# Kernel optimization log

Measured on AMD Instinct MI355X. Metric: run time of the kernel, lower is better.

## Reference

```python
import jax, jax.numpy as jnp
import numpy as np

# STDPConfig defaults
A_PLUS = 0.01
A_MINUS = 0.012
TAU_PLUS = 0.02
TAU_MINUS = 0.02
W_MIN = 0.0
W_MAX = 1.0
MAX_DT = 0.1
NEG_INF = -1e9  # stands in for -inf initial last-spike times (avoids inf-inf NaNs)


def setup_inputs() -> dict:
    key = jax.random.key(0)
    k1, k2, k3 = jax.random.split(key, 3)
    B, P, Q = 16, 2048, 2048
    pre_spikes = jax.random.bernoulli(k1, 0.05, (B, P)).astype(jnp.float32)
    post_spikes = jax.random.bernoulli(k2, 0.05, (B, Q)).astype(jnp.float32)
    # module initializes weights to a constant; randomize in [w_min, w_max] for a stronger test
    weights = jax.random.uniform(k3, (P, Q), jnp.float32, W_MIN, W_MAX)
    pre_trace = jnp.zeros((B, P), jnp.float32)
    post_trace = jnp.zeros((B, Q), jnp.float32)
    last_pre_spike = jnp.full((B, P), NEG_INF, jnp.float32)
    last_post_spike = jnp.full((B, Q), NEG_INF, jnp.float32)
    return {
        'pre_spikes': pre_spikes,
        'post_spikes': post_spikes,
        'weights': weights,
        'pre_trace': pre_trace,
        'post_trace': post_trace,
        'last_pre_spike': last_pre_spike,
        'last_post_spike': last_post_spike,
        'current_time': 0.5,
        'dt': 0.001,
    }


def reference(pre_spikes, post_spikes, weights, pre_trace, post_trace,
              last_pre_spike, last_post_spike, current_time, dt):
    # --- update last spike times ---
    pre_mask = pre_spikes > 0    # [B, P]
    post_mask = post_spikes > 0  # [B, Q]
    t_pre = jnp.where(pre_mask, current_time, last_pre_spike)    # [B, P]
    t_post = jnp.where(post_mask, current_time, last_post_spike)  # [B, Q]

    # --- trace decay + accumulation ---
    pre_trace_new = pre_trace * jnp.exp(jnp.float32(-dt / TAU_PLUS)) + pre_spikes
    post_trace_new = post_trace * jnp.exp(jnp.float32(-dt / TAU_MINUS)) + post_spikes

    # --- synaptic transmission ---
    synaptic_current = jnp.matmul(pre_spikes, weights)  # [B, Q]

    # --- vectorized STDP pairwise update (replaces the triple loop) ---
    # pair (i, j) is active iff pre i spiked AND post j spiked this step
    pair = pre_mask[:, :, None] & post_mask[:, None, :]              # [B, P, Q]
    dts = t_post[:, None, :] - t_pre[:, :, None]                     # post_time - pre_time
    dts = jnp.where(pair, dts, 0.0)                                  # mask out garbage (-inf diffs)
    ltp_cond = pair & (dts > 0) & (dts <= MAX_DT)
    ltd_cond = pair & (dts < 0) & (-dts <= MAX_DT)
    ltp = jnp.where(ltp_cond, A_PLUS * jnp.exp(-dts / TAU_PLUS), 0.0)
    ltd = jnp.where(ltd_cond, -A_MINUS * jnp.exp(dts / TAU_MINUS), 0.0)
    weight_changes = (ltp + ltd).mean(axis=0)                        # [P, Q]

    # --- multiplicative soft-bound update ---
    pot_change = weight_changes * (W_MAX - weights)
    dep_change = weight_changes * (weights - W_MIN)
    weight_update = jnp.where(weight_changes > 0, pot_change, dep_change)
    new_weights = jnp.clip(weights + weight_update, W_MIN, W_MAX)

    return (synaptic_current, weight_changes, pre_trace_new, post_trace_new, new_weights)
```

## Files before the change

kernel.cpp:

```cpp
#include <hip/hip_runtime.h>
#include <math.h>

#define B     16
#define PDIM  2048
#define QDIM  2048

#define NQB    8
#define NPC    64
#define PCHUNK 32

__global__ __launch_bounds__(256) void stdp_main(
    const float* __restrict__ pre_spikes,
    const float* __restrict__ weights,
    float* __restrict__ nw,
    float* __restrict__ wc,
    float* __restrict__ ws)
{
    __shared__ float sp[PCHUNK][B];

    const int qb   = blockIdx.x & (NQB - 1);
    const int pc   = blockIdx.x >> 3;
    const int p0   = pc * PCHUNK;
    const int wave = threadIdx.x >> 6;
    const int lane = threadIdx.x & 63;
    const int q    = qb * 256 + lane * 4;
    const int b0   = wave * 4;

    for (int t = threadIdx.x; t < B * PCHUNK; t += 256) {
        const int b  = t >> 5;
        const int pl = t & (PCHUNK - 1);
        sp[pl][b] = pre_spikes[b * PDIM + p0 + pl];
    }
    __syncthreads();

    float4 acc0 = {0,0,0,0}, acc1 = {0,0,0,0}, acc2 = {0,0,0,0}, acc3 = {0,0,0,0};

    const size_t base = (size_t)p0 * QDIM + q;
    const float* __restrict__ wp  = weights + base;
    float* __restrict__       nwp = nw + base;
    float* __restrict__       wcp = wc + base;

    #pragma unroll 8
    for (int i = 0; i < PCHUNK; ++i) {
        const float4 w = *(const float4*)(wp + (size_t)i * QDIM);
        const float4 s = *(const float4*)&sp[i][b0];

        acc0.x = fmaf(s.x, w.x, acc0.x); acc0.y = fmaf(s.x, w.y, acc0.y);
        acc0.z = fmaf(s.x, w.z, acc0.z); acc0.w = fmaf(s.x, w.w, acc0.w);
        acc1.x = fmaf(s.y, w.x, acc1.x); acc1.y = fmaf(s.y, w.y, acc1.y);
        acc1.z = fmaf(s.y, w.z, acc1.z); acc1.w = fmaf(s.y, w.w, acc1.w);
        acc2.x = fmaf(s.z, w.x, acc2.x); acc2.y = fmaf(s.z, w.y, acc2.y);
        acc2.z = fmaf(s.z, w.z, acc2.z); acc2.w = fmaf(s.z, w.w, acc2.w);
        acc3.x = fmaf(s.w, w.x, acc3.x); acc3.y = fmaf(s.w, w.y, acc3.y);
        acc3.z = fmaf(s.w, w.z, acc3.z); acc3.w = fmaf(s.w, w.w, acc3.w);

        if (wave == 0) {
            float4 c;
            c.x = fminf(fmaxf(w.x, 0.0f), 1.0f);
            c.y = fminf(fmaxf(w.y, 0.0f), 1.0f);
            c.z = fminf(fmaxf(w.z, 0.0f), 1.0f);
            c.w = fminf(fmaxf(w.w, 0.0f), 1.0f);
            *(float4*)(nwp + (size_t)i * QDIM) = c;
        } else if (wave == 1) {
            const float4 z = {0,0,0,0};
            *(float4*)(wcp + (size_t)i * QDIM) = z;
        }
    }

    float* __restrict__ wsp = ws + ((size_t)(pc * B + b0)) * QDIM + q;
    *(float4*)(wsp + 0 * (size_t)QDIM) = acc0;
    *(float4*)(wsp + 1 * (size_t)QDIM) = acc1;
    *(float4*)(wsp + 2 * (size_t)QDIM) = acc2;
    *(float4*)(wsp + 3 * (size_t)QDIM) = acc3;
}

__global__ __launch_bounds__(256) void stdp_tail(
    const float* __restrict__ pre_s,
    const float* __restrict__ post_s,
    const float* __restrict__ pre_t,
    const float* __restrict__ post_t,
    const float* __restrict__ dtp,
    const float* __restrict__ ws,
    float* __restrict__ pre_o,
    float* __restrict__ post_o,
    float* __restrict__ sc)
{
    const int i = blockIdx.x * blockDim.x + threadIdx.x;
    const float decay = expf(-dtp[0] * 50.0f);
    pre_o[i]  = pre_t[i]  * decay + pre_s[i];
    post_o[i] = post_t[i] * decay + post_s[i];

    if (i < (B * QDIM) / 4) {
        const int b  = i >> 9;
        const int qc = (i & 511) << 2;
        const float* __restrict__ p = ws + (size_t)b * QDIM + qc;
        float4 s = {0,0,0,0};
        #pragma unroll 8
        for (int pc = 0; pc < NPC; ++pc) {
            const float4 v = *(const float4*)(p + (size_t)pc * B * QDIM);
            s.x += v.x; s.y += v.y; s.z += v.z; s.w += v.w;
        }
        *(float4*)(sc + (size_t)b * QDIM + qc) = s;
    }
}

extern "C" void kernel_launch(void* const* d_in, const int* in_sizes, int n_in,
                              void* d_out, int out_size, void* d_ws, size_t ws_size,
                              hipStream_t stream) {
    const float* pre_spikes  = (const float*)d_in[0];
    const float* post_spikes = (const float*)d_in[1];
    const float* weights     = (const float*)d_in[2];
    const float* pre_trace   = (const float*)d_in[3];
    const float* post_trace  = (const float*)d_in[4];
    const float* dtp         = (const float*)d_in[8];

    float* out    = (float*)d_out;
    float* sc     = out;
    float* wc     = out + (size_t)B * QDIM;
    float* pre_o  = wc  + (size_t)PDIM * QDIM;
    float* post_o = pre_o + (size_t)B * PDIM;
    float* nw     = post_o + (size_t)B * QDIM;

    float* ws = (float*)d_ws;

    stdp_main<<<dim3(NQB * NPC), dim3(256), 0, stream>>>(
        pre_spikes, weights, nw, wc, ws);

    stdp_tail<<<dim3((B * PDIM) / 256), dim3(256), 0, stream>>>(
        pre_spikes, post_spikes, pre_trace, post_trace, dtp, ws, pre_o, post_o, sc);
}
```

Before: 101.9 us.

## Fuse trace update into main kernel and halve partial-sum chunks

```diff
diff --git a/kernel.cpp b/kernel.cpp
--- a/kernel.cpp
+++ b/kernel.cpp
@@ -6,15 +6,21 @@
 #define QDIM  2048
 
 #define NQB    8
-#define NPC    64
-#define PCHUNK 32
+#define NPC    32
+#define PCHUNK 64
 
-__global__ __launch_bounds__(256) void stdp_main(
+__global__ __launch_bounds__(512) void stdp_main(
     const float* __restrict__ pre_spikes,
+    const float* __restrict__ post_spikes,
+    const float* __restrict__ pre_trace,
+    const float* __restrict__ post_trace,
+    const float* __restrict__ dtp,
     const float* __restrict__ weights,
     float* __restrict__ nw,
     float* __restrict__ wc,
-    float* __restrict__ ws)
+    float* __restrict__ ws,
+    float* __restrict__ pre_o,
+    float* __restrict__ post_o)
 {
     __shared__ float sp[PCHUNK][B];
 
@@ -24,16 +30,39 @@
     const int wave = threadIdx.x >> 6;
     const int lane = threadIdx.x & 63;
     const int q    = qb * 256 + lane * 4;
-    const int b0   = wave * 4;
+    const int b0   = wave * 2;
 
-    for (int t = threadIdx.x; t < B * PCHUNK; t += 256) {
-        const int b  = t >> 5;
+    {
+        const int t = blockIdx.x * 512 + threadIdx.x;
+        if (t < 16384) {
+            const float decay = expf(-dtp[0] * 50.0f);
+            if (t < 8192) {
+                const float4 s = ((const float4*)pre_spikes)[t];
+                const float4 r = ((const float4*)pre_trace)[t];
+                float4 o;
+                o.x = fmaf(r.x, decay, s.x); o.y = fmaf(r.y, decay, s.y);
+                o.z = fmaf(r.z, decay, s.z); o.w = fmaf(r.w, decay, s.w);
+                ((float4*)pre_o)[t] = o;
+            } else {
+                const int u = t - 8192;
+                const float4 s = ((const float4*)post_spikes)[u];
+                const float4 r = ((const float4*)post_trace)[u];
+                float4 o;
+                o.x = fmaf(r.x, decay, s.x); o.y = fmaf(r.y, decay, s.y);
+                o.z = fmaf(r.z, decay, s.z); o.w = fmaf(r.w, decay, s.w);
+                ((float4*)post_o)[u] = o;
+            }
+        }
+    }
+
+    for (int t = threadIdx.x; t < B * PCHUNK; t += 512) {
+        const int b  = t >> 6;
         const int pl = t & (PCHUNK - 1);
         sp[pl][b] = pre_spikes[b * PDIM + p0 + pl];
     }
     __syncthreads();
 
-    float4 acc0 = {0,0,0,0}, acc1 = {0,0,0,0}, acc2 = {0,0,0,0}, acc3 = {0,0,0,0};
+    float4 acc0 = {0,0,0,0}, acc1 = {0,0,0,0};
 
     const size_t base = (size_t)p0 * QDIM + q;
     const float* __restrict__ wp  = weights + base;
@@ -43,16 +72,12 @@
     #pragma unroll 8
     for (int i = 0; i < PCHUNK; ++i) {
         const float4 w = *(const float4*)(wp + (size_t)i * QDIM);
-        const float4 s = *(const float4*)&sp[i][b0];
+        const float2 s = *(const float2*)&sp[i][b0];
 
         acc0.x = fmaf(s.x, w.x, acc0.x); acc0.y = fmaf(s.x, w.y, acc0.y);
         acc0.z = fmaf(s.x, w.z, acc0.z); acc0.w = fmaf(s.x, w.w, acc0.w);
         acc1.x = fmaf(s.y, w.x, acc1.x); acc1.y = fmaf(s.y, w.y, acc1.y);
         acc1.z = fmaf(s.y, w.z, acc1.z); acc1.w = fmaf(s.y, w.w, acc1.w);
-        acc2.x = fmaf(s.z, w.x, acc2.x); acc2.y = fmaf(s.z, w.y, acc2.y);
-        acc2.z = fmaf(s.z, w.z, acc2.z); acc2.w = fmaf(s.z, w.w, acc2.w);
-        acc3.x = fmaf(s.w, w.x, acc3.x); acc3.y = fmaf(s.w, w.y, acc3.y);
-        acc3.z = fmaf(s.w, w.z, acc3.z); acc3.w = fmaf(s.w, w.w, acc3.w);
 
         if (wave == 0) {
             float4 c;
@@ -70,38 +95,23 @@
     float* __restrict__ wsp = ws + ((size_t)(pc * B + b0)) * QDIM + q;
     *(float4*)(wsp + 0 * (size_t)QDIM) = acc0;
     *(float4*)(wsp + 1 * (size_t)QDIM) = acc1;
-    *(float4*)(wsp + 2 * (size_t)QDIM) = acc2;
-    *(float4*)(wsp + 3 * (size_t)QDIM) = acc3;
 }
 
-__global__ __launch_bounds__(256) void stdp_tail(
-    const float* __restrict__ pre_s,
-    const float* __restrict__ post_s,
-    const float* __restrict__ pre_t,
-    const float* __restrict__ post_t,
-    const float* __restrict__ dtp,
+__global__ __launch_bounds__(64) void stdp_screduce(
     const float* __restrict__ ws,
-    float* __restrict__ pre_o,
-    float* __restrict__ post_o,
     float* __restrict__ sc)
 {
-    const int i = blockIdx.x * blockDim.x + threadIdx.x;
-    const float decay = expf(-dtp[0] * 50.0f);
-    pre_o[i]  = pre_t[i]  * decay + pre_s[i];
-    post_o[i] = post_t[i] * decay + post_s[i];
-
-    if (i < (B * QDIM) / 4) {
-        const int b  = i >> 9;
-        const int qc = (i & 511) << 2;
-        const float* __restrict__ p = ws + (size_t)b * QDIM + qc;
-        float4 s = {0,0,0,0};
-        #pragma unroll 8
-        for (int pc = 0; pc < NPC; ++pc) {
-            const float4 v = *(const float4*)(p + (size_t)pc * B * QDIM);
-            s.x += v.x; s.y += v.y; s.z += v.z; s.w += v.w;
-        }
-        *(float4*)(sc + (size_t)b * QDIM + qc) = s;
+    const int u  = blockIdx.x * 64 + threadIdx.x;
+    const int b  = u >> 9;
+    const int qc = (u & 511) << 2;
+    const float* __restrict__ p = ws + (size_t)b * QDIM + qc;
+    float4 s = {0,0,0,0};
+    #pragma unroll
+    for (int pc = 0; pc < NPC; ++pc) {
+        const float4 v = *(const float4*)(p + (size_t)pc * B * QDIM);
+        s.x += v.x; s.y += v.y; s.z += v.z; s.w += v.w;
     }
+    *(float4*)(sc + (size_t)b * QDIM + qc) = s;
 }
 
 extern "C" void kernel_launch(void* const* d_in, const int* in_sizes, int n_in,
@@ -123,9 +133,9 @@
 
     float* ws = (float*)d_ws;
 
-    stdp_main<<<dim3(NQB * NPC), dim3(256), 0, stream>>>(
-        pre_spikes, weights, nw, wc, ws);
+    stdp_main<<<dim3(NQB * NPC), dim3(512), 0, stream>>>(
+        pre_spikes, post_spikes, pre_trace, post_trace, dtp, weights,
+        nw, wc, ws, pre_o, post_o);
 
-    stdp_tail<<<dim3((B * PDIM) / 256), dim3(256), 0, stream>>>(
-        pre_spikes, post_spikes, pre_trace, post_trace, dtp, ws, pre_o, post_o, sc);
+    stdp_screduce<<<dim3(128), dim3(64), 0, stream>>>(ws, sc);
 }
```

Measured after the change: 108.6 us. 6.5% more time.
